# Kernel optimization log

Hardware: AMD Instinct MI355X
Metric: run time of the kernel (lower is better)

## Reference

```python
import jax, jax.numpy as jnp
from jax import lax
import numpy as np

NUM_CLASSES = 80
SCORE_THR = 0.05
MIN_SIZE = 1.0
IOU_THR = 0.5
IMTOP = 100
PRE_NMS_K = 1000   # per-image candidate cap before NMS (jit-safe substitute for dynamic nonzero filtering)
N_IMG = 2
BBOX_CLIP = float(np.log(1000.0 / 16.0))  # standard dw/dh clamp in decode_boxes(clamp=True)


def setup_inputs() -> dict:
    key = jax.random.key(0)
    ks = jax.random.split(key, 12)
    R, C, S, CLIN = 2000, 256, 7, 1024
    c1 = C * S * S
    roi_maps = jax.random.normal(ks[0], (R, C, S, S), jnp.float32) * 0.1
    xy = jax.random.uniform(ks[1], (R, 2), jnp.float32, 0.0, 600.0)
    wh = jax.random.uniform(ks[2], (R, 2), jnp.float32, 8.0, 200.0)
    proposals = jnp.concatenate([xy, xy + wh], axis=-1)  # valid xyxy boxes
    imidx = jnp.sort(jax.random.randint(ks[3], (R,), 0, N_IMG)).astype(jnp.int32)
    imsizes = jnp.full((N_IMG, 2), 800.0, jnp.float32)  # (h, w) per image
    def lin(k, o, i):
        return jax.random.normal(k, (o, i), jnp.float32) * (1.0 / np.sqrt(i))
    return {
        'roi_maps': roi_maps, 'proposals': proposals, 'imidx': imidx, 'imsizes': imsizes,
        'fc1_w': lin(ks[4], CLIN, c1), 'fc1_b': jnp.zeros((CLIN,), jnp.float32),
        'fc2_w': lin(ks[5], CLIN, CLIN), 'fc2_b': jnp.zeros((CLIN,), jnp.float32),
        'cls_w': lin(ks[6], 1 + NUM_CLASSES, CLIN), 'cls_b': jnp.zeros((1 + NUM_CLASSES,), jnp.float32),
        'reg_w': lin(ks[7], NUM_CLASSES * 4, CLIN), 'reg_b': jnp.zeros((NUM_CLASSES * 4,), jnp.float32),
    }


def _nms_single(boxes, scores, cls):
    # boxes [K,4] xyxy (sorted by score desc), scores [K] (-1 = invalid), cls [K]
    K = scores.shape[0]
    valid = scores > 0.0
    # batched_nms trick: offset boxes by class so different classes never overlap
    off = cls.astype(boxes.dtype) * (jnp.max(boxes) + 1.0)
    ob = boxes + off[:, None]
    x1, y1, x2, y2 = ob[:, 0], ob[:, 1], ob[:, 2], ob[:, 3]
    area = (x2 - x1) * (y2 - y1)
    iw = jnp.clip(jnp.minimum(x2[:, None], x2[None, :]) - jnp.maximum(x1[:, None], x1[None, :]), 0.0)
    ih = jnp.clip(jnp.minimum(y2[:, None], y2[None, :]) - jnp.maximum(y1[:, None], y1[None, :]), 0.0)
    inter = iw * ih
    iou = inter / (area[:, None] + area[None, :] - inter + 1e-9)  # [K,K]
    ar = jnp.arange(K)

    def body(i, carry):
        sup, keep = carry
        k = jnp.logical_not(sup[i])
        keep = keep.at[i].set(k)
        sup = sup | (k & (iou[i] > IOU_THR) & (ar > i))
        return (sup, keep)

    sup, keep = lax.fori_loop(0, K, body, (jnp.logical_not(valid), jnp.zeros((K,), bool)))
    order = jnp.sort(jnp.where(keep, ar, K))[:IMTOP]
    vo = order < K
    idx = jnp.minimum(order, K - 1)
    b = jnp.where(vo[:, None], boxes[idx], 0.0)
    s = jnp.where(vo, scores[idx], 0.0)
    c = jnp.where(vo, cls[idx], -1)
    return b, s, c


def _forward(roi_maps, proposals, imsizes, fc1_w, fc1_b, fc2_w, fc2_b,
             cls_w, cls_b, reg_w, reg_b, imidx):
    R = roi_maps.shape[0]
    x = roi_maps.reshape(R, -1)
    x = jax.nn.relu(x @ fc1_w.T + fc1_b)
    x = jax.nn.relu(x @ fc2_w.T + fc2_b)
    reg = (x @ reg_w.T + reg_b).reshape(R, NUM_CLASSES, 4)  # per-class deltas
    logit = x @ cls_w.T + cls_b                              # [R, 1+C]
    scr = jax.nn.softmax(logit, axis=-1)[:, :-1]             # bckg_class_first=False -> drop last
    # convert_to_cwh
    pw = proposals[:, 2] - proposals[:, 0]
    ph = proposals[:, 3] - proposals[:, 1]
    pcx = proposals[:, 0] + 0.5 * pw
    pcy = proposals[:, 1] + 0.5 * ph
    # decode_boxes, mults=(0.1, 0.2), clamp dw/dh
    dx = reg[..., 0] * 0.1
    dy = reg[..., 1] * 0.1
    dw = jnp.minimum(reg[..., 2] * 0.2, BBOX_CLIP)
    dh = jnp.minimum(reg[..., 3] * 0.2, BBOX_CLIP)
    cx = dx * pw[:, None] + pcx[:, None]
    cy = dy * ph[:, None] + pcy[:, None]
    w = jnp.exp(dw) * pw[:, None]
    h = jnp.exp(dh) * ph[:, None]
    boxes = jnp.stack([cx - 0.5 * w, cy - 0.5 * h, cx + 0.5 * w, cy + 0.5 * h], axis=-1)  # [R,C,4]
    # clamp_to_canvas: imsizes is (h, w)
    sz = imsizes[imidx]  # [R,2]
    maxs = jnp.stack([sz[:, 1], sz[:, 0], sz[:, 1], sz[:, 0]], axis=-1)[:, None, :]
    boxes = jnp.clip(boxes, 0.0, maxs)
    bw = boxes[..., 2] - boxes[..., 0]
    bh = boxes[..., 3] - boxes[..., 1]
    # score_thr filter + remove_small, expressed as score masking (jit-safe)
    mask = (scr > SCORE_THR) & (bw >= MIN_SIZE) & (bh >= MIN_SIZE)
    scores = jnp.where(mask, scr, -1.0)  # [R,C]
    flat_boxes = boxes.reshape(-1, 4)
    flat_cls = jnp.broadcast_to(jnp.arange(NUM_CLASSES), (R, NUM_CLASSES)).reshape(-1)
    # per-image candidate scores, pre-NMS top-K
    img_mask = imidx[None, :] == jnp.arange(N_IMG)[:, None]            # [N,R]
    img_scores = jnp.where(img_mask[:, :, None], scores[None], -1.0).reshape(N_IMG, -1)
    top_s, top_i = lax.top_k(img_scores, PRE_NMS_K)                    # [N,K]
    b_k = flat_boxes[top_i]                                            # [N,K,4]
    c_k = flat_cls[top_i]                                              # [N,K]
    return jax.vmap(_nms_single)(b_k, top_s, c_k)


def reference(roi_maps, proposals, imidx, imsizes, fc1_w, fc1_b, fc2_w, fc2_b,
              cls_w, cls_b, reg_w, reg_b):
    return _forward(roi_maps, proposals, imsizes, fc1_w, fc1_b, fc2_w, fc2_b,
                    cls_w, cls_b, reg_w, reg_b, imidx)
```

## Files before the change

kernel.cpp:

```cpp
#include <hip/hip_runtime.h>
#include <cstdint>

typedef unsigned int u32;
typedef unsigned long long u64;
typedef _Float16 f16;
typedef f16 f16x8 __attribute__((ext_vector_type(8)));
typedef f16 f16x4 __attribute__((ext_vector_type(4)));
typedef float f32x4 __attribute__((ext_vector_type(4)));

#define R_ROIS 2000
#define CIN 12544
#define HID 1024
#define NCLS 80
#define NHEAD 401
#define RC (R_ROIS*NCLS)
#define KTOP 1000
#define IMTOP 100
#define KEY_NEG1 0x407FFFFFu
#define BBOX_CLIPV 4.135166556742356f
#define NCHUNK 157

__device__ __forceinline__ u32 fkey(float f) {
  u32 u = __float_as_uint(f);
  return (u & 0x80000000u) ? ~u : (u | 0x80000000u);
}
__device__ __forceinline__ float fkeyinv(u32 k) {
  u32 b = (k & 0x80000000u) ? (k & 0x7FFFFFFFu) : ~k;
  return __uint_as_float(b);
}
__device__ __forceinline__ u32 mkey(const u32* keys, const int* imidx, int i, int g) {
  int r = i / NCLS;
  return (imidx[r] == g) ? keys[i] : KEY_NEG1;
}

__device__ __forceinline__ void lds16(const f16* gsrc, f16* ldst) {
  __builtin_amdgcn_global_load_lds(
      (const __attribute__((address_space(1))) void*)gsrc,
      (__attribute__((address_space(3))) void*)ldst, 16, 0, 0);
}

__global__ __launch_bounds__(256, 2)
void gemm_f16x3(const f16* __restrict__ A1, const f16* __restrict__ A2,
                const f16* __restrict__ B1, const f16* __restrict__ B2,
                float* __restrict__ C, int M, int N, int K, int kLen)
{
  __shared__ __align__(16) f16 As1[128 * 32];
  __shared__ __align__(16) f16 As2[128 * 32];
  __shared__ __align__(16) f16 Bs1[128 * 32];
  __shared__ __align__(16) f16 Bs2[128 * 32];

  int t = threadIdx.x;
  int w = t >> 6, lane = t & 63;
  int wm = w >> 1, wn = w & 1;
  int m0 = blockIdx.y * 128, n0 = blockIdx.x * 128;
  int k0 = blockIdx.z * kLen;

  f32x4 acc[4][4];
#pragma unroll
  for (int mi = 0; mi < 4; ++mi)
#pragma unroll
    for (int ni = 0; ni < 4; ++ni)
#pragma unroll
      for (int r = 0; r < 4; ++r) acc[mi][ni][r] = 0.f;

  int row0 = t >> 2,           off0 = (t & 3) * 8;
  int row1 = (t + 256) >> 2,   off1 = ((t + 256) & 3) * 8;
  int rmA0 = m0 + row0; if (rmA0 > M - 1) rmA0 = M - 1;
  int rmA1 = m0 + row1; if (rmA1 > M - 1) rmA1 = M - 1;
  size_t a0 = (size_t)rmA0 * K + off0, a1 = (size_t)rmA1 * K + off1;
  size_t b0 = (size_t)(n0 + row0) * K + off0, b1 = (size_t)(n0 + row1) * K + off1;
  int sw0 = (w * 64) * 8;
  int sw1 = (256 + w * 64) * 8;

  int rrow = lane & 15;
  int rsel = (lane >> 4) * 8;

  for (int ks = 0; ks < kLen; ks += 32) {
    int kb = k0 + ks;
    lds16(A1 + a0 + kb, As1 + sw0);  lds16(A1 + a1 + kb, As1 + sw1);
    lds16(A2 + a0 + kb, As2 + sw0);  lds16(A2 + a1 + kb, As2 + sw1);
    lds16(B1 + b0 + kb, Bs1 + sw0);  lds16(B1 + b1 + kb, Bs1 + sw1);
    lds16(B2 + b0 + kb, Bs2 + sw0);  lds16(B2 + b1 + kb, Bs2 + sw1);
    __syncthreads();

    f16x8 af1[4], af2[4], bf1[4], bf2[4];
#pragma unroll
    for (int mi = 0; mi < 4; ++mi) {
      int ra = (wm * 64 + mi * 16 + rrow) * 32 + rsel;
      af1[mi] = *(const f16x8*)&As1[ra];
      af2[mi] = *(const f16x8*)&As2[ra];
    }
#pragma unroll
    for (int ni = 0; ni < 4; ++ni) {
      int rb = (wn * 64 + ni * 16 + rrow) * 32 + rsel;
      bf1[ni] = *(const f16x8*)&Bs1[rb];
      bf2[ni] = *(const f16x8*)&Bs2[rb];
    }
#pragma unroll
    for (int mi = 0; mi < 4; ++mi)
#pragma unroll
      for (int ni = 0; ni < 4; ++ni) {
        acc[mi][ni] = __builtin_amdgcn_mfma_f32_16x16x32_f16(af1[mi], bf1[ni], acc[mi][ni], 0, 0, 0);
        acc[mi][ni] = __builtin_amdgcn_mfma_f32_16x16x32_f16(af1[mi], bf2[ni], acc[mi][ni], 0, 0, 0);
        acc[mi][ni] = __builtin_amdgcn_mfma_f32_16x16x32_f16(af2[mi], bf1[ni], acc[mi][ni], 0, 0, 0);
      }
    __syncthreads();
  }

  int crow = m0 + wm * 64 + (lane >> 4) * 4;
  int ccol = n0 + wn * 64 + (lane & 15);
#pragma unroll
  for (int mi = 0; mi < 4; ++mi)
#pragma unroll
    for (int r = 0; r < 4; ++r) {
      int rm = crow + mi * 16 + r;
      if (rm < M) {
#pragma unroll
        for (int ni = 0; ni < 4; ++ni)
          atomicAdd(&C[(size_t)rm * N + ccol + ni * 16], acc[mi][ni][r]);
      }
    }
}

__global__ void split_fp16_k(const float* __restrict__ X, f16* __restrict__ H1,
                             f16* __restrict__ H2, int total4)
{
  int i4 = blockIdx.x * blockDim.x + threadIdx.x;
  if (i4 >= total4) return;
  float4 v = ((const float4*)X)[i4];
  f16x4 o1, o2;
  float x;
  x = v.x; o1[0] = (f16)x; o2[0] = (f16)(x - (float)o1[0]);
  x = v.y; o1[1] = (f16)x; o2[1] = (f16)(x - (float)o1[1]);
  x = v.z; o1[2] = (f16)x; o2[2] = (f16)(x - (float)o1[2]);
  x = v.w; o1[3] = (f16)x; o2[3] = (f16)(x - (float)o1[3]);
  ((f16x4*)H1)[i4] = o1;
  ((f16x4*)H2)[i4] = o2;
}

__global__ void bias_relu_split_k(const float* __restrict__ X, const float* __restrict__ bias,
                                  f16* __restrict__ H1, f16* __restrict__ H2, int total)
{
  int i = blockIdx.x * blockDim.x + threadIdx.x;
  if (i >= total) return;
  float v = fmaxf(X[i] + bias[i & (HID - 1)], 0.f);
  f16 a = (f16)v;
  H1[i] = a;
  H2[i] = (f16)(v - (float)a);
}

__global__ __launch_bounds__(256, 2)
void gemm128(const float* __restrict__ A, int lda,
             const float* __restrict__ B, int ldb,
             float* __restrict__ C, int M, int N, int kLen)
{
  __shared__ float As[128][20];
  __shared__ float Bs[128][20];
  int t = threadIdx.x;
  int tx = t & 15, ty = t >> 4;
  int m0 = blockIdx.y * 128, n0 = blockIdx.x * 128;
  int k0 = blockIdx.z * kLen;
  float acc[8][8];
#pragma unroll
  for (int i = 0; i < 8; ++i)
#pragma unroll
    for (int j = 0; j < 8; ++j) acc[i][j] = 0.f;

  int lr = t >> 2;
  int lk = (t & 3) * 4;

  for (int ks = 0; ks < kLen; ks += 16) {
#pragma unroll
    for (int p = 0; p < 2; ++p) {
      int row = lr + p * 64;
      int rm = m0 + row; if (rm > M - 1) rm = M - 1;
      float4 av = *(const float4*)(A + (size_t)rm * lda + k0 + ks + lk);
      *(float4*)&As[row][lk] = av;
      int rn = n0 + row; if (rn > N - 1) rn = N - 1;
      float4 bv = *(const float4*)(B + (size_t)rn * ldb + k0 + ks + lk);
      *(float4*)&Bs[row][lk] = bv;
    }
    __syncthreads();
#pragma unroll
    for (int kk = 0; kk < 16; kk += 4) {
      float4 a4[8], b4[8];
#pragma unroll
      for (int i = 0; i < 8; ++i) a4[i] = *(const float4*)&As[ty + (i << 4)][kk];
#pragma unroll
      for (int j = 0; j < 8; ++j) b4[j] = *(const float4*)&Bs[tx + (j << 4)][kk];
#pragma unroll
      for (int i = 0; i < 8; ++i)
#pragma unroll
        for (int j = 0; j < 8; ++j) {
          acc[i][j] += a4[i].x * b4[j].x;
          acc[i][j] += a4[i].y * b4[j].y;
          acc[i][j] += a4[i].z * b4[j].z;
          acc[i][j] += a4[i].w * b4[j].w;
        }
    }
    __syncthreads();
  }
#pragma unroll
  for (int i = 0; i < 8; ++i) {
    int rm = m0 + ty + (i << 4);
    if (rm < M) {
#pragma unroll
      for (int j = 0; j < 8; ++j) {
        int rn = n0 + tx + (j << 4);
        atomicAdd(&C[(size_t)rm * N + rn], acc[i][j]);
      }
    }
  }
}

__global__ void bias_relu_k(float* __restrict__ X, const float* __restrict__ bias, int total4)
{
  int i4 = blockIdx.x * blockDim.x + threadIdx.x;
  if (i4 >= total4) return;
  int c4 = i4 & 255;
  float4 v = ((float4*)X)[i4];
  float4 b = ((const float4*)bias)[c4];
  v.x = fmaxf(v.x + b.x, 0.f);
  v.y = fmaxf(v.y + b.y, 0.f);
  v.z = fmaxf(v.z + b.z, 0.f);
  v.w = fmaxf(v.w + b.w, 0.f);
  ((float4*)X)[i4] = v;
}

__global__ __launch_bounds__(256)
void gemm_heads(const float* __restrict__ A,
                const float* __restrict__ clsw, const float* __restrict__ clsb,
                const float* __restrict__ regw, const float* __restrict__ regb,
                float* __restrict__ H)
{
  __shared__ float As[64][36];
  __shared__ float Bs[64][36];
  int t = threadIdx.x;
  int tx = t & 15, ty = t >> 4;
  int m0 = blockIdx.y * 64, n0 = blockIdx.x * 64;
  float acc[4][4] = {};
  int lr = t >> 3;
  int lk = (t & 7) * 4;

  for (int ks = 0; ks < HID; ks += 32) {
#pragma unroll
    for (int p = 0; p < 2; ++p) {
      int row = lr + p * 32;
      int rm = m0 + row; if (rm > R_ROIS - 1) rm = R_ROIS - 1;
      *(float4*)&As[row][lk] = *(const float4*)(A + (size_t)rm * HID + ks + lk);
      int rn = n0 + row; if (rn > NHEAD - 1) rn = NHEAD - 1;
      const float* bp = (rn < 81) ? (clsw + (size_t)rn * HID) : (regw + (size_t)(rn - 81) * HID);
      *(float4*)&Bs[row][lk] = *(const float4*)(bp + ks + lk);
    }
    __syncthreads();
#pragma unroll
    for (int kk = 0; kk < 32; kk += 4) {
      float4 a4[4], b4[4];
#pragma unroll
      for (int i = 0; i < 4; ++i) a4[i] = *(const float4*)&As[ty + (i << 4)][kk];
#pragma unroll
      for (int j = 0; j < 4; ++j) b4[j] = *(const float4*)&Bs[tx + (j << 4)][kk];
#pragma unroll
      for (int i = 0; i < 4; ++i)
#pragma unroll
        for (int j = 0; j < 4; ++j) {
          acc[i][j] += a4[i].x * b4[j].x;
          acc[i][j] += a4[i].y * b4[j].y;
          acc[i][j] += a4[i].z * b4[j].z;
          acc[i][j] += a4[i].w * b4[j].w;
        }
    }
    __syncthreads();
  }
#pragma unroll
  for (int i = 0; i < 4; ++i) {
    int rm = m0 + ty + (i << 4);
#pragma unroll
    for (int j = 0; j < 4; ++j) {
      int rn = n0 + tx + (j << 4);
      if (rm < R_ROIS && rn < NHEAD) {
        float b = (rn < 81) ? clsb[rn] : regb[rn - 81];
        H[(size_t)rm * NHEAD + rn] = acc[i][j] + b;
      }
    }
  }
}

__global__ __launch_bounds__(256)
void decode_k(const float* __restrict__ H, const float* __restrict__ prop,
              const int* __restrict__ imidx, const float* __restrict__ imsz,
              u32* __restrict__ keys, float* __restrict__ boxes)
{
  int lane = threadIdx.x & 63;
  int r = blockIdx.x * 4 + (threadIdx.x >> 6);
  const float* h = H + (size_t)r * NHEAD;
  float l0 = h[lane];
  float l1 = (lane < 17) ? h[64 + lane] : -1e30f;
  float mx = fmaxf(l0, l1);
#pragma unroll
  for (int o = 32; o; o >>= 1) mx = fmaxf(mx, __shfl_xor(mx, o));
  float e0 = expf(l0 - mx);
  float e1 = (lane < 17) ? expf(l1 - mx) : 0.f;
  float s = e0 + e1;
#pragma unroll
  for (int o = 32; o; o >>= 1) s += __shfl_xor(s, o);

  float px1 = prop[r * 4 + 0], py1 = prop[r * 4 + 1];
  float px2 = prop[r * 4 + 2], py2 = prop[r * 4 + 3];
  float pw = px2 - px1, ph = py2 - py1;
  float pcx = px1 + 0.5f * pw, pcy = py1 + 0.5f * ph;
  int g = imidx[r];
  float imh = imsz[g * 2 + 0], imw = imsz[g * 2 + 1];

#pragma unroll
  for (int q = 0; q < 2; ++q) {
    int c = (q == 0) ? lane : 64 + lane;
    bool on = (q == 0) ? true : (lane < 16);
    if (on) {
      float e = (q == 0) ? e0 : e1;
      float scr = e / s;
      const float* rg = h + 81 + c * 4;
      float dx = rg[0] * 0.1f, dy = rg[1] * 0.1f;
      float dw = fminf(rg[2] * 0.2f, BBOX_CLIPV);
      float dh = fminf(rg[3] * 0.2f, BBOX_CLIPV);
      float cx = dx * pw + pcx, cy = dy * ph + pcy;
      float w = expf(dw) * pw, hh = expf(dh) * ph;
      float x1 = cx - 0.5f * w, y1 = cy - 0.5f * hh;
      float x2 = cx + 0.5f * w, y2 = cy + 0.5f * hh;
      x1 = fminf(fmaxf(x1, 0.f), imw);
      x2 = fminf(fmaxf(x2, 0.f), imw);
      y1 = fminf(fmaxf(y1, 0.f), imh);
      y2 = fminf(fmaxf(y2, 0.f), imh);
      float bw = x2 - x1, bh = y2 - y1;
      bool msk = (scr > 0.05f) && (bw >= 1.f) && (bh >= 1.f);
      float sm = msk ? scr : -1.f;
      int idx = r * 80 + c;
      keys[idx] = fkey(sm);
      ((float4*)boxes)[idx] = make_float4(x1, y1, x2, y2);
    }
  }
}

__global__ void hist_k(const u32* __restrict__ keys, const int* __restrict__ imidx,
                       const u32* __restrict__ sel, u32* __restrict__ hist, int level, int nbins)
{
  __shared__ u32 lh[2048];
  int t = threadIdx.x, g = blockIdx.y;
  for (int b = t; b < 2048; b += 256) lh[b] = 0;
  __syncthreads();
  u32 b1 = 0, pre21 = 0;
  if (level == 2) b1 = sel[g * 8 + 0];
  if (level == 3) pre21 = (sel[g * 8 + 0] << 11) | sel[g * 8 + 1];
  for (int i = blockIdx.x * 256 + t; i < RC; i += gridDim.x * 256) {
    u32 k = mkey(keys, imidx, i, g);
    if (level == 1) atomicAdd(&lh[k >> 21], 1u);
    else if (level == 2) { if ((k >> 21) == b1) atomicAdd(&lh[(k >> 10) & 0x7FFu], 1u); }
    else { if ((k >> 10) == pre21) atomicAdd(&lh[k & 0x3FFu], 1u); }
  }
  __syncthreads();
  for (int b = t; b < nbins; b += 256) { u32 v = lh[b]; if (v) atomicAdd(&hist[g * nbins + b], v); }
}

__global__ void find_k(const u32* __restrict__ hist, int nbins, u32* __restrict__ sel, int level)
{
  __shared__ u32 sh[256];
  int t = threadIdx.x, g = blockIdx.x;
  int per = nbins >> 8;
  const u32* h = hist + g * nbins;
  u32 mySum = 0;
  for (int jj = 0; jj < per; ++jj) mySum += h[t * per + jj];
  u32 base = (level == 1) ? 0u : sel[g * 8 + 3];
  sh[t] = mySum; __syncthreads();
  for (int off = 1; off < 256; off <<= 1) {
    u32 v = (t + off < 256) ? sh[t + off] : 0u; __syncthreads();
    sh[t] += v; __syncthreads();
  }
  u32 c = base + ((t < 255) ? sh[t + 1] : 0u);
  for (int jj = per - 1; jj >= 0; --jj) {
    int b = t * per + jj;
    u32 cnt = h[b];
    if (c < KTOP && c + cnt >= KTOP) {
      if (level == 1) { sel[g * 8 + 0] = (u32)b; sel[g * 8 + 3] = c; }
      else if (level == 2) { sel[g * 8 + 1] = (u32)b; sel[g * 8 + 3] = c; }
      else {
        u32 T = (sel[g * 8 + 0] << 21) | (sel[g * 8 + 1] << 10) | (u32)b;
        sel[g * 8 + 4] = T; sel[g * 8 + 3] = c; sel[g * 8 + 5] = KTOP - c;
      }
    }
    c += cnt;
  }
}

__global__ void eqcount_k(const u32* __restrict__ keys, const int* __restrict__ imidx,
                          const u32* __restrict__ sel, u32* __restrict__ eqcnt)
{
  int g = blockIdx.y, t = threadIdx.x;
  int i = blockIdx.x * 1024 + t;
  u32 T = sel[g * 8 + 4];
  bool eq = (i < RC) && (mkey(keys, imidx, i, g) == T);
  u64 bal = __ballot(eq);
  __shared__ u32 wc[16];
  if ((t & 63) == 0) wc[t >> 6] = (u32)__popcll(bal);
  __syncthreads();
  if (t == 0) {
    u32 sum = 0;
    for (int w = 0; w < 16; ++w) sum += wc[w];
    eqcnt[g * 160 + blockIdx.x] = sum;
  }
}

__global__ void eqscan_k(const u32* __restrict__ eqcnt, u32* __restrict__ eqoff)
{
  __shared__ u32 sh[256];
  int t = threadIdx.x, g = blockIdx.x;
  u32 v = (t < NCHUNK) ? eqcnt[g * 160 + t] : 0u;
  sh[t] = v; __syncthreads();
  for (int off = 1; off < 256; off <<= 1) {
    u32 u = (t >= off) ? sh[t - off] : 0u; __syncthreads();
    sh[t] += u; __syncthreads();
  }
  if (t < NCHUNK) eqoff[g * 160 + t] = sh[t] - v;
}

__global__ void emit_k(const u32* __restrict__ keys, const int* __restrict__ imidx,
                       const u32* __restrict__ sel, const u32* __restrict__ eqoff,
                       u32* __restrict__ cntgt, u32* __restrict__ cand)
{
  int g = blockIdx.y, t = threadIdx.x;
  int i = blockIdx.x * 1024 + t;
  u32 T = sel[g * 8 + 4], m = sel[g * 8 + 5], ra = sel[g * 8 + 3];
  u32 k = (i < RC) ? mkey(keys, imidx, i, g) : 0u;
  if (k > T) { u32 p = atomicAdd(&cntgt[g], 1u); cand[g * 1024 + p] = (u32)i; }
  bool eq = (k == T);
  u64 bal = __ballot(eq);
  int w = t >> 6, lane = t & 63;
  __shared__ u32 wc[16];
  if (lane == 0) wc[w] = (u32)__popcll(bal);
  __syncthreads();
  u32 wb = 0;
  for (int x = 0; x < w; ++x) wb += wc[x];
  if (eq) {
    u32 lanePre = (u32)__popcll(bal & ((1ull << lane) - 1ull));
    u32 rank = eqoff[g * 160 + blockIdx.x] + wb + lanePre;
    if (rank < m) cand[g * 1024 + ra + rank] = (u32)i;
  }
}

__global__ __launch_bounds__(512)
void sort_k(const u32* __restrict__ cand, const u32* __restrict__ keys,
            const int* __restrict__ imidx, u64* __restrict__ sorted)
{
  __shared__ u64 sm[1024];
  int t = threadIdx.x, g = blockIdx.x;
#pragma unroll
  for (int p = 0; p < 2; ++p) {
    int s = t + p * 512;
    u64 e = ~0ull;
    if (s < KTOP) {
      u32 i = cand[g * 1024 + s];
      u32 k = mkey(keys, imidx, (int)i, g);
      e = ((u64)(~k) << 32) | (u64)i;
    }
    sm[s] = e;
  }
  __syncthreads();
  for (int kk = 2; kk <= 1024; kk <<= 1)
    for (int j = kk >> 1; j > 0; j >>= 1) {
#pragma unroll
      for (int p = 0; p < 2; ++p) {
        int i = t + p * 512;
        int ixj = i ^ j;
        if (ixj > i) {
          u64 a = sm[i], b = sm[ixj];
          bool up = ((i & kk) == 0);
          if ((a > b) == up) { sm[i] = b; sm[ixj] = a; }
        }
      }
      __syncthreads();
    }
  sorted[g * 1024 + t] = sm[t];
  sorted[g * 1024 + t + 512] = sm[t + 512];
}

__global__ void gather1_k(const u64* __restrict__ sorted, const float* __restrict__ boxes,
                          u32* __restrict__ idx_k, float* __restrict__ sc_k,
                          float4* __restrict__ box_k, u64* __restrict__ inval, u32* __restrict__ maxbits)
{
  int t = threadIdx.x, g = blockIdx.x;
  u64 e = sorted[g * 1024 + t];
  u32 idx = (u32)e;
  u32 k = ~(u32)(e >> 32);
  float sc = fkeyinv(k);
  bool val = (t < KTOP) && (sc > 0.f);
  if (t < KTOP) {
    idx_k[g * 1024 + t] = idx;
    sc_k[g * 1024 + t] = sc;
    float4 b = ((const float4*)boxes)[idx];
    box_k[g * 1024 + t] = b;
    u32 m1 = __float_as_uint(b.x) > __float_as_uint(b.y) ? __float_as_uint(b.x) : __float_as_uint(b.y);
    u32 m2 = __float_as_uint(b.z) > __float_as_uint(b.w) ? __float_as_uint(b.z) : __float_as_uint(b.w);
    atomicMax(&maxbits[g], m1 > m2 ? m1 : m2);
  }
  u64 bal = __ballot(!val);
  if ((t & 63) == 0) inval[g * 16 + (t >> 6)] = bal;
}

__global__ void gather2_k(const u32* __restrict__ idx_k, const float4* __restrict__ box_k,
                          const u32* __restrict__ maxbits, float4* __restrict__ ob, float* __restrict__ area)
{
  int t = threadIdx.x, g = blockIdx.x;
  if (t >= KTOP) return;
  float mx = __uint_as_float(maxbits[g]);
  u32 idx = idx_k[g * 1024 + t];
  float off = (float)(idx % NCLS) * (mx + 1.0f);
  float4 b = box_k[g * 1024 + t];
  float4 o = make_float4(b.x + off, b.y + off, b.z + off, b.w + off);
  ob[g * 1024 + t] = o;
  area[g * 1024 + t] = (o.z - o.x) * (o.w - o.y);
}

__global__ __launch_bounds__(256)
void nmsmat_k(const float4* __restrict__ ob, const float* __restrict__ area, u64* __restrict__ Mrow)
{
  __shared__ float4 sob[KTOP];
  __shared__ float sar[KTOP];
  int t = threadIdx.x, g = blockIdx.y;
  for (int s = t; s < KTOP; s += 256) { sob[s] = ob[g * 1024 + s]; sar[s] = area[g * 1024 + s]; }
  __syncthreads();
  int w = blockIdx.x * 256 + t;
  if (w >= KTOP * 16) return;
  int i = w >> 4, jw = w & 15;
  float4 bi = sob[i];
  float ai = sar[i];
  u64 bits = 0;
  int jbase = jw * 64;
  for (int b = 0; b < 64; ++b) {
    int j = jbase + b;
    if (j < KTOP && j > i) {
      float4 bj = sob[j];
      float iw = fminf(bi.z, bj.z) - fmaxf(bi.x, bj.x); iw = fmaxf(iw, 0.f);
      float ih = fminf(bi.w, bj.w) - fmaxf(bi.y, bj.y); ih = fmaxf(ih, 0.f);
      float inter = iw * ih;
      float iou = inter / (ai + sar[j] - inter + 1e-9f);
      if (iou > 0.5f) bits |= (1ull << b);
    }
  }
  Mrow[(size_t)(g * KTOP + i) * 16 + jw] = bits;
}

__global__ void nmsscan_k(const u64* __restrict__ Mrow, const u64* __restrict__ inval,
                          const u32* __restrict__ idx_k, const float* __restrict__ sc_k,
                          const float4* __restrict__ box_k, float* __restrict__ out)
{
  int lane = threadIdx.x;
  int g = blockIdx.x;
  u64 remv = (lane < 16) ? inval[g * 16 + lane] : 0ull;
  __shared__ int keepL[IMTOP];
  int nk = 0;
  for (int i = 0; i < KTOP; ++i) {
    int wd = i >> 6;
    u64 rw = __shfl(remv, wd);
    if (!((rw >> (i & 63)) & 1ull)) {
      if (lane < 16) remv |= Mrow[(size_t)(g * KTOP + i) * 16 + lane];
      if (lane == 0) keepL[nk] = i;
      ++nk;
      if (nk == IMTOP) break;
    }
  }
  __syncthreads();
  for (int s = lane; s < IMTOP; s += 64) {
    float4 b = make_float4(0.f, 0.f, 0.f, 0.f);
    float sc = 0.f, cf = -1.f;
    if (s < nk) {
      int i = keepL[s];
      b = box_k[g * 1024 + i];
      sc = sc_k[g * 1024 + i];
      cf = (float)(idx_k[g * 1024 + i] % NCLS);
    }
    ((float4*)out)[g * IMTOP + s] = b;
    out[800 + g * IMTOP + s] = sc;
    out[1000 + g * IMTOP + s] = cf;
  }
}

extern "C" void kernel_launch(void* const* d_in, const int* in_sizes, int n_in,
                              void* d_out, int out_size, void* d_ws, size_t ws_size,
                              hipStream_t stream) {
  (void)in_sizes; (void)n_in; (void)out_size;
  const float* roi  = (const float*)d_in[0];
  const float* prop = (const float*)d_in[1];
  const int*   imix = (const int*)d_in[2];
  const float* imsz = (const float*)d_in[3];
  const float* fc1w = (const float*)d_in[4];
  const float* fc1b = (const float*)d_in[5];
  const float* fc2w = (const float*)d_in[6];
  const float* fc2b = (const float*)d_in[7];
  const float* clsw = (const float*)d_in[8];
  const float* clsb = (const float*)d_in[9];
  const float* regw = (const float*)d_in[10];
  const float* regb = (const float*)d_in[11];
  float* out = (float*)d_out;

  char* ws = (char*)d_ws;
  size_t o = 0;
  auto alloc = [&](size_t bytes) { size_t r = o; o += (bytes + 255) & ~(size_t)255; return r; };
  float* C1    = (float*)(ws + alloc((size_t)R_ROIS * HID * 4));
  float* C2    = (float*)(ws + alloc((size_t)R_ROIS * HID * 4));
  float* HEADS = (float*)(ws + alloc((size_t)R_ROIS * NHEAD * 4));
  u32*   KEYS  = (u32*)  (ws + alloc((size_t)RC * 4));
  float* BOXES = (float*)(ws + alloc((size_t)RC * 16));
  u64*   MROW  = (u64*)  (ws + alloc((size_t)2 * KTOP * 16 * 8));
  u64*   SORTED= (u64*)  (ws + alloc(2 * 1024 * 8));
  u32*   CAND  = (u32*)  (ws + alloc(2 * 1024 * 4));
  u32*   IDXK  = (u32*)  (ws + alloc(2 * 1024 * 4));
  float* SCK   = (float*)(ws + alloc(2 * 1024 * 4));
  float4* BOXK = (float4*)(ws + alloc(2 * 1024 * 16));
  float4* OBK  = (float4*)(ws + alloc(2 * 1024 * 16));
  float* AREA  = (float*)(ws + alloc(2 * 1024 * 4));
  u64*   INVAL = (u64*)  (ws + alloc(2 * 16 * 8));
  size_t zz0 = o;
  u32* HIST1 = (u32*)(ws + alloc(2 * 2048 * 4));
  u32* HIST2 = (u32*)(ws + alloc(2 * 2048 * 4));
  u32* HIST3 = (u32*)(ws + alloc(2 * 1024 * 4));
  u32* SEL   = (u32*)(ws + alloc(2 * 8 * 4));
  u32* CNTGT = (u32*)(ws + alloc(2 * 4));
  u32* MAXB  = (u32*)(ws + alloc(2 * 4));
  size_t zzBytes = o - zz0;
  u32* EQCNT = (u32*)(ws + alloc(2 * 160 * 4));
  u32* EQOFF = (u32*)(ws + alloc(2 * 160 * 4));

  f16* A1h = (f16*)(ws + alloc((size_t)R_ROIS * CIN * 2));
  f16* A2h = (f16*)(ws + alloc((size_t)R_ROIS * CIN * 2));
  f16* B1h = (f16*)(ws + alloc((size_t)HID * CIN * 2));
  f16* B2h = (f16*)(ws + alloc((size_t)HID * CIN * 2));
  f16* X1h = (f16*)(ws + alloc((size_t)R_ROIS * HID * 2));
  f16* X2h = (f16*)(ws + alloc((size_t)R_ROIS * HID * 2));
  f16* W1h = (f16*)(ws + alloc((size_t)HID * HID * 2));
  f16* W2h = (f16*)(ws + alloc((size_t)HID * HID * 2));
  bool fp16ok = (o <= ws_size);

  hipMemsetAsync(C1, 0, (size_t)2 * R_ROIS * HID * 4, stream);
  hipMemsetAsync(ws + zz0, 0, zzBytes, stream);

  if (fp16ok) {
    int nro4 = R_ROIS * CIN / 4, nw14 = HID * CIN / 4, nw24 = HID * HID / 4;
    split_fp16_k<<<(nro4 + 255) / 256, 256, 0, stream>>>(roi, A1h, A2h, nro4);
    split_fp16_k<<<(nw14 + 255) / 256, 256, 0, stream>>>(fc1w, B1h, B2h, nw14);
    split_fp16_k<<<(nw24 + 255) / 256, 256, 0, stream>>>(fc2w, W1h, W2h, nw24);
    gemm_f16x3<<<dim3(8, 16, 4), 256, 0, stream>>>(A1h, A2h, B1h, B2h, C1, R_ROIS, HID, CIN, 3136);
    bias_relu_split_k<<<(R_ROIS * HID + 255) / 256, 256, 0, stream>>>(C1, fc1b, X1h, X2h, R_ROIS * HID);
    gemm_f16x3<<<dim3(8, 16, 4), 256, 0, stream>>>(X1h, X2h, W1h, W2h, C2, R_ROIS, HID, HID, 256);
    bias_relu_k<<<2000, 256, 0, stream>>>(C2, fc2b, R_ROIS * HID / 4);
  } else {
    gemm128<<<dim3(8, 16, 4), 256, 0, stream>>>(roi, CIN, fc1w, CIN, C1, R_ROIS, HID, 3136);
    bias_relu_k<<<2000, 256, 0, stream>>>(C1, fc1b, R_ROIS * HID / 4);
    gemm128<<<dim3(8, 16, 4), 256, 0, stream>>>(C1, HID, fc2w, HID, C2, R_ROIS, HID, 256);
    bias_relu_k<<<2000, 256, 0, stream>>>(C2, fc2b, R_ROIS * HID / 4);
  }
  gemm_heads<<<dim3(7, 32), 256, 0, stream>>>(C2, clsw, clsb, regw, regb, HEADS);
  decode_k<<<500, 256, 0, stream>>>(HEADS, prop, imix, imsz, KEYS, BOXES);
  hist_k<<<dim3(128, 2), 256, 0, stream>>>(KEYS, imix, SEL, HIST1, 1, 2048);
  find_k<<<2, 256, 0, stream>>>(HIST1, 2048, SEL, 1);
  hist_k<<<dim3(128, 2), 256, 0, stream>>>(KEYS, imix, SEL, HIST2, 2, 2048);
  find_k<<<2, 256, 0, stream>>>(HIST2, 2048, SEL, 2);
  hist_k<<<dim3(128, 2), 256, 0, stream>>>(KEYS, imix, SEL, HIST3, 3, 1024);
  find_k<<<2, 256, 0, stream>>>(HIST3, 1024, SEL, 3);
  eqcount_k<<<dim3(NCHUNK, 2), 1024, 0, stream>>>(KEYS, imix, SEL, EQCNT);
  eqscan_k<<<2, 256, 0, stream>>>(EQCNT, EQOFF);
  emit_k<<<dim3(NCHUNK, 2), 1024, 0, stream>>>(KEYS, imix, SEL, EQOFF, CNTGT, CAND);
  sort_k<<<2, 512, 0, stream>>>(CAND, KEYS, imix, SORTED);
  gather1_k<<<2, 1024, 0, stream>>>(SORTED, BOXES, IDXK, SCK, BOXK, INVAL, MAXB);
  gather2_k<<<2, 1024, 0, stream>>>(IDXK, BOXK, MAXB, OBK, AREA);
  nmsmat_k<<<dim3(63, 2), 256, 0, stream>>>(OBK, AREA, MROW);
  nmsscan_k<<<2, 64, 0, stream>>>(MROW, INVAL, IDXK, SCK, BOXK, out);
}
```

Measured before the change: 675.6 us.

## Double-buffer fp16x3 GEMM, swizzle LDS, move head GEMM to MFMA, fuse small kernels

The split-fp16 MFMA GEMM now double-buffers its LDS tiles so the next K-slice's global-to-LDS loads overlap compute. It also XOR-swizzles LDS columns to reduce bank conflicts and raises wave priority around the MFMA block. The classifier and regression head GEMM now runs on the same fp16x3 kernel, with packed head weights and a bias-prefilled output, replacing the fp32 gemm_heads path. The three fp32-to-fp16 split kernels are merged into one grid-stride launch, and the two gather kernels are fused using a shared-memory max. The cost is double the LDS per block, which may lower occupancy, plus extra workspace and conversion work for the heads.

```diff
diff --git a/kernel.cpp b/kernel.cpp
--- a/kernel.cpp
+++ b/kernel.cpp
@@ -44,10 +44,10 @@
                 const f16* __restrict__ B1, const f16* __restrict__ B2,
                 float* __restrict__ C, int M, int N, int K, int kLen)
 {
-  __shared__ __align__(16) f16 As1[128 * 32];
-  __shared__ __align__(16) f16 As2[128 * 32];
-  __shared__ __align__(16) f16 Bs1[128 * 32];
-  __shared__ __align__(16) f16 Bs2[128 * 32];
+  __shared__ __align__(16) f16 As1[2][128 * 32];
+  __shared__ __align__(16) f16 As2[2][128 * 32];
+  __shared__ __align__(16) f16 Bs1[2][128 * 32];
+  __shared__ __align__(16) f16 Bs2[2][128 * 32];
 
   int t = threadIdx.x;
   int w = t >> 6, lane = t & 63;
@@ -63,39 +63,60 @@
 #pragma unroll
       for (int r = 0; r < 4; ++r) acc[mi][ni][r] = 0.f;
 
-  int row0 = t >> 2,           off0 = (t & 3) * 8;
-  int row1 = (t + 256) >> 2,   off1 = ((t + 256) & 3) * 8;
+  int row0 = t >> 2;       int j0 = (t & 3) ^ ((row0 >> 1) & 3);
+  int t1r  = t + 256;
+  int row1 = t1r >> 2;     int j1 = (t1r & 3) ^ ((row1 >> 1) & 3);
   int rmA0 = m0 + row0; if (rmA0 > M - 1) rmA0 = M - 1;
   int rmA1 = m0 + row1; if (rmA1 > M - 1) rmA1 = M - 1;
-  size_t a0 = (size_t)rmA0 * K + off0, a1 = (size_t)rmA1 * K + off1;
-  size_t b0 = (size_t)(n0 + row0) * K + off0, b1 = (size_t)(n0 + row1) * K + off1;
+  int rnB0 = n0 + row0; if (rnB0 > N - 1) rnB0 = N - 1;
+  int rnB1 = n0 + row1; if (rnB1 > N - 1) rnB1 = N - 1;
+  size_t a0 = (size_t)rmA0 * K + j0 * 8, a1 = (size_t)rmA1 * K + j1 * 8;
+  size_t b0 = (size_t)rnB0 * K + j0 * 8, b1 = (size_t)rnB1 * K + j1 * 8;
   int sw0 = (w * 64) * 8;
   int sw1 = (256 + w * 64) * 8;
 
   int rrow = lane & 15;
-  int rsel = (lane >> 4) * 8;
-
-  for (int ks = 0; ks < kLen; ks += 32) {
-    int kb = k0 + ks;
-    lds16(A1 + a0 + kb, As1 + sw0);  lds16(A1 + a1 + kb, As1 + sw1);
-    lds16(A2 + a0 + kb, As2 + sw0);  lds16(A2 + a1 + kb, As2 + sw1);
-    lds16(B1 + b0 + kb, Bs1 + sw0);  lds16(B1 + b1 + kb, Bs1 + sw1);
-    lds16(B2 + b0 + kb, Bs2 + sw0);  lds16(B2 + b1 + kb, Bs2 + sw1);
-    __syncthreads();
+  int cxor = (rrow >> 1) & 3;
+  int rsel = ((lane >> 4) ^ cxor) * 8;
+
+  int nt = kLen / 32;
+  {
+    int kb = k0;
+    lds16(A1 + a0 + kb, &As1[0][sw0]); lds16(A1 + a1 + kb, &As1[0][sw1]);
+    lds16(A2 + a0 + kb, &As2[0][sw0]); lds16(A2 + a1 + kb, &As2[0][sw1]);
+    lds16(B1 + b0 + kb, &Bs1[0][sw0]); lds16(B1 + b1 + kb, &Bs1[0][sw1]);
+    lds16(B2 + b0 + kb, &Bs2[0][sw0]); lds16(B2 + b1 + kb, &Bs2[0][sw1]);
+  }
+  asm volatile("s_waitcnt vmcnt(0)" ::: "memory");
+  __builtin_amdgcn_s_barrier();
+  __builtin_amdgcn_sched_barrier(0);
+
+  int cur = 0;
+  for (int tt = 0; tt < nt; ++tt) {
+    if (tt + 1 < nt) {
+      int kb = k0 + (tt + 1) * 32;
+      int nx = cur ^ 1;
+      lds16(A1 + a0 + kb, &As1[nx][sw0]); lds16(A1 + a1 + kb, &As1[nx][sw1]);
+      lds16(A2 + a0 + kb, &As2[nx][sw0]); lds16(A2 + a1 + kb, &As2[nx][sw1]);
+      lds16(B1 + b0 + kb, &Bs1[nx][sw0]); lds16(B1 + b1 + kb, &Bs1[nx][sw1]);
+      lds16(B2 + b0 + kb, &Bs2[nx][sw0]); lds16(B2 + b1 + kb, &Bs2[nx][sw1]);
+    }
+    __builtin_amdgcn_sched_barrier(0);
 
     f16x8 af1[4], af2[4], bf1[4], bf2[4];
 #pragma unroll
     for (int mi = 0; mi < 4; ++mi) {
       int ra = (wm * 64 + mi * 16 + rrow) * 32 + rsel;
-      af1[mi] = *(const f16x8*)&As1[ra];
-      af2[mi] = *(const f16x8*)&As2[ra];
+      af1[mi] = *(const f16x8*)&As1[cur][ra];
+      af2[mi] = *(const f16x8*)&As2[cur][ra];
     }
 #pragma unroll
     for (int ni = 0; ni < 4; ++ni) {
       int rb = (wn * 64 + ni * 16 + rrow) * 32 + rsel;
-      bf1[ni] = *(const f16x8*)&Bs1[rb];
-      bf2[ni] = *(const f16x8*)&Bs2[rb];
-    }
+      bf1[ni] = *(const f16x8*)&Bs1[cur][rb];
+      bf2[ni] = *(const f16x8*)&Bs2[cur][rb];
+    }
+    __builtin_amdgcn_s_setprio(1);
 #pragma unroll
     for (int mi = 0; mi < 4; ++mi)
 #pragma unroll
@@ -104,7 +125,12 @@
         acc[mi][ni] = __builtin_amdgcn_mfma_f32_16x16x32_f16(af1[mi], bf2[ni], acc[mi][ni], 0, 0, 0);
         acc[mi][ni] = __builtin_amdgcn_mfma_f32_16x16x32_f16(af2[mi], bf1[ni], acc[mi][ni], 0, 0, 0);
       }
-    __syncthreads();
+    __builtin_amdgcn_s_setprio(0);
+    __builtin_amdgcn_sched_barrier(0);
+    asm volatile("s_waitcnt vmcnt(0)" ::: "memory");
+    __builtin_amdgcn_s_barrier();
+    __builtin_amdgcn_sched_barrier(0);
+    cur ^= 1;
   }
 
   int crow = m0 + wm * 64 + (lane >> 4) * 4;
@@ -116,26 +142,63 @@
       int rm = crow + mi * 16 + r;
       if (rm < M) {
 #pragma unroll
-        for (int ni = 0; ni < 4; ++ni)
-          atomicAdd(&C[(size_t)rm * N + ccol + ni * 16], acc[mi][ni][r]);
+        for (int ni = 0; ni < 4; ++ni) {
+          int cc = ccol + ni * 16;
+          if (cc < N) atomicAdd(&C[(size_t)rm * N + cc], acc[mi][ni][r]);
+        }
       }
     }
 }
 
-__global__ void split_fp16_k(const float* __restrict__ X, f16* __restrict__ H1,
-                             f16* __restrict__ H2, int total4)
-{
-  int i4 = blockIdx.x * blockDim.x + threadIdx.x;
-  if (i4 >= total4) return;
-  float4 v = ((const float4*)X)[i4];
+__global__ void split3_k(const float* __restrict__ s0, int c0,
+                         const float* __restrict__ s1, int c1,
+                         const float* __restrict__ s2, int c2,
+                         f16* __restrict__ d0a, f16* __restrict__ d0b,
+                         f16* __restrict__ d1a, f16* __restrict__ d1b,
+                         f16* __restrict__ d2a, f16* __restrict__ d2b)
+{
+  int total = c0 + c1 + c2;
+  for (int i = blockIdx.x * blockDim.x + threadIdx.x; i < total; i += gridDim.x * blockDim.x) {
+    const float* src; f16 *da, *db; int j;
+    if (i < c0) { src = s0; da = d0a; db = d0b; j = i; }
+    else if (i < c0 + c1) { src = s1; da = d1a; db = d1b; j = i - c0; }
+    else { src = s2; da = d2a; db = d2b; j = i - c0 - c1; }
+    float4 v = ((const float4*)src)[j];
+    f16x4 o1, o2;
+    o1[0] = (f16)v.x; o2[0] = (f16)(v.x - (float)o1[0]);
+    o1[1] = (f16)v.y; o2[1] = (f16)(v.y - (float)o1[1]);
+    o1[2] = (f16)v.z; o2[2] = (f16)(v.z - (float)o1[2]);
+    o1[3] = (f16)v.w; o2[3] = (f16)(v.w - (float)o1[3]);
+    ((f16x4*)da)[j] = o1;
+    ((f16x4*)db)[j] = o2;
+  }
+}
+
+__global__ void packhead_k(const float* __restrict__ clsw, const float* __restrict__ regw,
+                           f16* __restrict__ W1, f16* __restrict__ W2)
+{
+  int i = blockIdx.x * blockDim.x + threadIdx.x;
+  if (i >= 512 * 256) return;
+  int r = i >> 8, c4 = i & 255;
+  int rr = (r < NHEAD) ? r : (NHEAD - 1);
+  const float* src = (rr < 81) ? (clsw + (size_t)rr * HID) : (regw + (size_t)(rr - 81) * HID);
+  float4 v = ((const float4*)src)[c4];
   f16x4 o1, o2;
-  float x;
-  x = v.x; o1[0] = (f16)x; o2[0] = (f16)(x - (float)o1[0]);
-  x = v.y; o1[1] = (f16)x; o2[1] = (f16)(x - (float)o1[1]);
-  x = v.z; o1[2] = (f16)x; o2[2] = (f16)(x - (float)o1[2]);
-  x = v.w; o1[3] = (f16)x; o2[3] = (f16)(x - (float)o1[3]);
-  ((f16x4*)H1)[i4] = o1;
-  ((f16x4*)H2)[i4] = o2;
+  o1[0] = (f16)v.x; o2[0] = (f16)(v.x - (float)o1[0]);
+  o1[1] = (f16)v.y; o2[1] = (f16)(v.y - (float)o1[1]);
+  o1[2] = (f16)v.z; o2[2] = (f16)(v.z - (float)o1[2]);
+  o1[3] = (f16)v.w; o2[3] = (f16)(v.w - (float)o1[3]);
+  ((f16x4*)W1)[i] = o1;
+  ((f16x4*)W2)[i] = o2;
+}
+
+__global__ void biasfill_k(const float* __restrict__ clsb, const float* __restrict__ regb,
+                           float* __restrict__ H)
+{
+  int i = blockIdx.x * blockDim.x + threadIdx.x;
+  if (i >= R_ROIS * NHEAD) return;
+  int c = i % NHEAD;
+  H[i] = (c < 81) ? clsb[c] : regb[c - 81];
 }
 
 __global__ void bias_relu_split_k(const float* __restrict__ X, const float* __restrict__ bias,
@@ -482,41 +545,40 @@
   sorted[g * 1024 + t + 512] = sm[t + 512];
 }
 
-__global__ void gather1_k(const u64* __restrict__ sorted, const float* __restrict__ boxes,
-                          u32* __restrict__ idx_k, float* __restrict__ sc_k,
-                          float4* __restrict__ box_k, u64* __restrict__ inval, u32* __restrict__ maxbits)
-{
+__global__ void gather_k(const u64* __restrict__ sorted, const float* __restrict__ boxes,
+                         u32* __restrict__ idx_k, float* __restrict__ sc_k,
+                         float4* __restrict__ box_k, u64* __restrict__ inval,
+                         float4* __restrict__ ob, float* __restrict__ area)
+{
+  __shared__ u32 smax;
   int t = threadIdx.x, g = blockIdx.x;
+  if (t == 0) smax = 0;
+  __syncthreads();
   u64 e = sorted[g * 1024 + t];
   u32 idx = (u32)e;
   u32 k = ~(u32)(e >> 32);
   float sc = fkeyinv(k);
   bool val = (t < KTOP) && (sc > 0.f);
+  float4 b = make_float4(0.f, 0.f, 0.f, 0.f);
   if (t < KTOP) {
     idx_k[g * 1024 + t] = idx;
     sc_k[g * 1024 + t] = sc;
-    float4 b = ((const float4*)boxes)[idx];
+    b = ((const float4*)boxes)[idx];
     box_k[g * 1024 + t] = b;
     u32 m1 = __float_as_uint(b.x) > __float_as_uint(b.y) ? __float_as_uint(b.x) : __float_as_uint(b.y);
     u32 m2 = __float_as_uint(b.z) > __float_as_uint(b.w) ? __float_as_uint(b.z) : __float_as_uint(b.w);
-    atomicMax(&maxbits[g], m1 > m2 ? m1 : m2);
+    atomicMax(&smax, m1 > m2 ? m1 : m2);
   }
   u64 bal = __ballot(!val);
   if ((t & 63) == 0) inval[g * 16 + (t >> 6)] = bal;
-}
-
-__global__ void gather2_k(const u32* __restrict__ idx_k, const float4* __restrict__ box_k,
-                          const u32* __restrict__ maxbits, float4* __restrict__ ob, float* __restrict__ area)
-{
-  int t = threadIdx.x, g = blockIdx.x;
-  if (t >= KTOP) return;
-  float mx = __uint_as_float(maxbits[g]);
-  u32 idx = idx_k[g * 1024 + t];
-  float off = (float)(idx % NCLS) * (mx + 1.0f);
-  float4 b = box_k[g * 1024 + t];
-  float4 o = make_float4(b.x + off, b.y + off, b.z + off, b.w + off);
-  ob[g * 1024 + t] = o;
-  area[g * 1024 + t] = (o.z - o.x) * (o.w - o.y);
+  __syncthreads();
+  float mx = __uint_as_float(smax);
+  if (t < KTOP) {
+    float off = (float)(idx % NCLS) * (mx + 1.0f);
+    float4 o = make_float4(b.x + off, b.y + off, b.z + off, b.w + off);
+    ob[g * 1024 + t] = o;
+    area[g * 1024 + t] = (o.z - o.x) * (o.w - o.y);
+  }
 }
 
 __global__ __launch_bounds__(256)
@@ -624,7 +686,6 @@
   u32* HIST3 = (u32*)(ws + alloc(2 * 1024 * 4));
   u32* SEL   = (u32*)(ws + alloc(2 * 8 * 4));
   u32* CNTGT = (u32*)(ws + alloc(2 * 4));
-  u32* MAXB  = (u32*)(ws + alloc(2 * 4));
   size_t zzBytes = o - zz0;
   u32* EQCNT = (u32*)(ws + alloc(2 * 160 * 4));
   u32* EQOFF = (u32*)(ws + alloc(2 * 160 * 4));
@@ -637,27 +698,33 @@
   f16* X2h = (f16*)(ws + alloc((size_t)R_ROIS * HID * 2));
   f16* W1h = (f16*)(ws + alloc((size_t)HID * HID * 2));
   f16* W2h = (f16*)(ws + alloc((size_t)HID * HID * 2));
+  f16* Y1h = (f16*)(ws + alloc((size_t)R_ROIS * HID * 2));
+  f16* Y2h = (f16*)(ws + alloc((size_t)R_ROIS * HID * 2));
+  f16* WH1 = (f16*)(ws + alloc((size_t)512 * HID * 2));
+  f16* WH2 = (f16*)(ws + alloc((size_t)512 * HID * 2));
   bool fp16ok = (o <= ws_size);
 
   hipMemsetAsync(C1, 0, (size_t)2 * R_ROIS * HID * 4, stream);
   hipMemsetAsync(ws + zz0, 0, zzBytes, stream);
 
   if (fp16ok) {
-    int nro4 = R_ROIS * CIN / 4, nw14 = HID * CIN / 4, nw24 = HID * HID / 4;
-    split_fp16_k<<<(nro4 + 255) / 256, 256, 0, stream>>>(roi, A1h, A2h, nro4);
-    split_fp16_k<<<(nw14 + 255) / 256, 256, 0, stream>>>(fc1w, B1h, B2h, nw14);
-    split_fp16_k<<<(nw24 + 255) / 256, 256, 0, stream>>>(fc2w, W1h, W2h, nw24);
+    split3_k<<<2048, 256, 0, stream>>>(roi, R_ROIS * CIN / 4, fc1w, HID * CIN / 4,
+                                       fc2w, HID * HID / 4,
+                                       A1h, A2h, B1h, B2h, W1h, W2h);
+    packhead_k<<<512, 256, 0, stream>>>(clsw, regw, WH1, WH2);
+    biasfill_k<<<(R_ROIS * NHEAD + 255) / 256, 256, 0, stream>>>(clsb, regb, HEADS);
     gemm_f16x3<<<dim3(8, 16, 4), 256, 0, stream>>>(A1h, A2h, B1h, B2h, C1, R_ROIS, HID, CIN, 3136);
     bias_relu_split_k<<<(R_ROIS * HID + 255) / 256, 256, 0, stream>>>(C1, fc1b, X1h, X2h, R_ROIS * HID);
     gemm_f16x3<<<dim3(8, 16, 4), 256, 0, stream>>>(X1h, X2h, W1h, W2h, C2, R_ROIS, HID, HID, 256);
-    bias_relu_k<<<2000, 256, 0, stream>>>(C2, fc2b, R_ROIS * HID / 4);
+    bias_relu_split_k<<<(R_ROIS * HID + 255) / 256, 256, 0, stream>>>(C2, fc2b, Y1h, Y2h, R_ROIS * HID);
+    gemm_f16x3<<<dim3(4, 16, 4), 256, 0, stream>>>(Y1h, Y2h, WH1, WH2, HEADS, R_ROIS, NHEAD, HID, 256);
   } else {
     gemm128<<<dim3(8, 16, 4), 256, 0, stream>>>(roi, CIN, fc1w, CIN, C1, R_ROIS, HID, 3136);
     bias_relu_k<<<2000, 256, 0, stream>>>(C1, fc1b, R_ROIS * HID / 4);
     gemm128<<<dim3(8, 16, 4), 256, 0, stream>>>(C1, HID, fc2w, HID, C2, R_ROIS, HID, 256);
     bias_relu_k<<<2000, 256, 0, stream>>>(C2, fc2b, R_ROIS * HID / 4);
-  }
-  gemm_heads<<<dim3(7, 32), 256, 0, stream>>>(C2, clsw, clsb, regw, regb, HEADS);
+    gemm_heads<<<dim3(7, 32), 256, 0, stream>>>(C2, clsw, clsb, regw, regb, HEADS);
+  }
   decode_k<<<500, 256, 0, stream>>>(HEADS, prop, imix, imsz, KEYS, BOXES);
   hist_k<<<dim3(128, 2), 256, 0, stream>>>(KEYS, imix, SEL, HIST1, 1, 2048);
   find_k<<<2, 256, 0, stream>>>(HIST1, 2048, SEL, 1);
@@ -669,8 +736,7 @@
   eqscan_k<<<2, 256, 0, stream>>>(EQCNT, EQOFF);
   emit_k<<<dim3(NCHUNK, 2), 1024, 0, stream>>>(KEYS, imix, SEL, EQOFF, CNTGT, CAND);
   sort_k<<<2, 512, 0, stream>>>(CAND, KEYS, imix, SORTED);
-  gather1_k<<<2, 1024, 0, stream>>>(SORTED, BOXES, IDXK, SCK, BOXK, INVAL, MAXB);
-  gather2_k<<<2, 1024, 0, stream>>>(IDXK, BOXK, MAXB, OBK, AREA);
+  gather_k<<<2, 1024, 0, stream>>>(SORTED, BOXES, IDXK, SCK, BOXK, INVAL, OBK, AREA);
   nmsmat_k<<<dim3(63, 2), 256, 0, stream>>>(OBK, AREA, MROW);
   nmsscan_k<<<2, 64, 0, stream>>>(MROW, INVAL, IDXK, SCK, BOXK, out);
 }
```

New measurement: 651.4 us. -3.6%, faster.
